# Performance work log

Measured on AMD Instinct MI355X. Metric: run time of the kernel, lower is better.

## Reference

```python
import jax, jax.numpy as jnp
from jax import lax
import numpy as np

B, CIN, HC, K, REC = 64, 64, 64, 3, 5
MG = 240 // REC  # 48
EPS = 1e-8


def conv2d(x, w, b, pad):
    y = lax.conv_general_dilated(x, w, (1, 1), [(pad, pad), (pad, pad)],
                                 dimension_numbers=('NCHW', 'OIHW', 'NCHW'))
    return y + b[None, :, None, None]


def conv_transpose2d(x, w, b, stride, pad):
    # PyTorch ConvTranspose2d: w is (Cin, Cout, kH, kW)
    k = w.shape[2]
    w_t = jnp.transpose(w[:, :, ::-1, ::-1], (1, 0, 2, 3))  # -> OIHW, flipped
    y = lax.conv_general_dilated(x, w_t, (1, 1),
                                 [(k - 1 - pad, k - 1 - pad)] * 2,
                                 lhs_dilation=(stride, stride),
                                 dimension_numbers=('NCHW', 'OIHW', 'NCHW'))
    return y + b[None, :, None, None]


def leaky(x):
    return jnp.where(x >= 0, x, 0.2 * x)


def setup_inputs() -> dict:
    key = jax.random.key(0)
    ks = jax.random.split(key, 12)
    s = 0.05
    return {
        'x': jax.random.normal(ks[0], (B, CIN, 64, 64), jnp.float32),
        'h': jax.random.normal(ks[1], (B, HC, 64, 64), jnp.float32),
        'c': jax.random.normal(ks[2], (B, HC, 64, 64), jnp.float32),
        'recalled_memory_feature': jax.random.normal(ks[3], (B, REC, MG, 32, 32), jnp.float32),
        'conv_w': jax.random.normal(ks[4], (5 * HC, CIN + HC, K, K), jnp.float32) * s,
        'conv_b': jax.random.normal(ks[5], (5 * HC,), jnp.float32) * s,
        'convc_w': jax.random.normal(ks[6], (MG, HC, 1, 1), jnp.float32) * s,
        'convc_b': jax.random.normal(ks[7], (MG,), jnp.float32) * s,
        'convssm_w': jax.random.normal(ks[8], (MG, MG, 4, 4), jnp.float32) * s,
        'convssm_b': jax.random.normal(ks[9], (MG,), jnp.float32) * s,
        'convfuse_w': jax.random.normal(ks[10], (HC, MG + HC, 1, 1), jnp.float32) * s,
        'convfuse_b': jax.random.normal(ks[11], (HC,), jnp.float32) * s,
    }


def reference(x, h, c, recalled_memory_feature, conv_w, conv_b, convc_w, convc_b,
              convssm_w, convssm_b, convfuse_w, convfuse_b):
    rm = recalled_memory_feature.reshape(B, REC, MG, 32, 32)
    rm_avg = rm.mean(axis=(3, 4))                      # (B, REC, MG)
    q = leaky(conv2d(c, convc_w, convc_b, 0))          # (B, MG, 64, 64)
    q_avg = q.mean(axis=(2, 3))                        # (B, MG)
    # cosine similarity along channel dim, vectorized over (B, REC)
    qn = jnp.maximum(jnp.linalg.norm(q_avg, axis=1, keepdims=True), EPS)   # (B,1)
    mn = jnp.maximum(jnp.linalg.norm(rm_avg, axis=2), EPS)                  # (B,REC)
    cos = jnp.einsum('bm,brm->br', q_avg, rm_avg) / (qn * mn)               # (B,REC)
    attn = jax.nn.softmax(cos, axis=1)                                      # (B,REC)
    mt = jnp.einsum('br,brmhw->bmhw', attn, rm)        # (B, MG, 32, 32)
    mt = leaky(conv_transpose2d(mt, convssm_w, convssm_b, 2, 1))  # (B, MG, 64, 64)

    gates = conv2d(jnp.concatenate((x, h), axis=1), conv_w, conv_b, K // 2)
    i, f, g, o, lam = jnp.split(gates, 5, axis=1)
    i = jax.nn.sigmoid(i)
    f = jax.nn.sigmoid(f)
    o = jax.nn.sigmoid(o)
    g = jnp.tanh(g)
    lam = jax.nn.sigmoid(lam)
    c_new = f * c + i * g
    h_new = o * jnp.tanh(conv2d(jnp.concatenate((c_new, mt), axis=1), convfuse_w, convfuse_b, 0))
    h_out = lam * h_new + (1.0 - lam) * h
    return (h_out, c_new)
```

## Files before the change

### kernel.cpp

```cpp
#include <hip/hip_runtime.h>
#include <hip/hip_bf16.h>
#include <cstdint>

#define HW 4096
#define MGc 48
#define RECc 5

typedef __attribute__((ext_vector_type(8))) short bf16x8;
typedef __attribute__((ext_vector_type(4))) float f32x4;

__device__ __forceinline__ float sigf(float x) { return 1.f / (1.f + expf(-x)); }
__device__ __forceinline__ float leakyf(float x) { return x >= 0.f ? x : 0.2f * x; }
__device__ __forceinline__ unsigned short f2bfu(float f) {
  __hip_bfloat16 b = __float2bfloat16(f);
  return *reinterpret_cast<unsigned short*>(&b);
}
__device__ __forceinline__ float bfu2f(unsigned short u) {
  unsigned v = ((unsigned)u) << 16;
  return __uint_as_float(v);
}
__device__ __forceinline__ void gload_lds16(const void* g, void* l) {
  __builtin_amdgcn_global_load_lds(
      (const __attribute__((address_space(1))) unsigned int*)g,
      (__attribute__((address_space(3))) unsigned int*)l, 16, 0, 0);
}

__global__ __launch_bounds__(256) void k_head(const float* __restrict__ cw,
    __hip_bfloat16* __restrict__ Wp, __hip_bfloat16* __restrict__ Pp,
    const float* __restrict__ xin, const float* __restrict__ hin,
    const float* __restrict__ rm, float* __restrict__ rm_sum,
    const float* __restrict__ c, const float* __restrict__ ccw,
    const float* __restrict__ ccb, float* __restrict__ q_part) {
  __shared__ __align__(16) char smem[16704];
  int bid = blockIdx.x;
  int tid = threadIdx.x;
  if (bid < 1440) {
    int idx = bid * 256 + tid;
    int t = idx / (320 * 128);
    int rem = idx % (320 * 128);
    int ocp = rem / 128, ci = rem % 128;
    int nt = ocp / 80, r2 = ocp % 80, gate = r2 / 16, ml = r2 % 16;
    int oc = gate * 64 + nt * 16 + ml;
    Wp[idx] = __float2bfloat16(cw[((size_t)oc * 128 + ci) * 9 + t]);
  } else if (bid < 2480) {
    int idx = (bid - 1440) * 256 + tid;
    int b = idx / 4160, i = idx % 4160;
    bf16x8* base = reinterpret_cast<bf16x8*>(Pp);
    size_t u;
    if (i < 2112) {
      int r = (i < 1056) ? 0 : 65;
      int j = (i < 1056) ? i : i - 1056;
      u = ((size_t)b * 66 + r) * 1056 + j;
    } else {
      int i2 = i - 2112;
      int row = 1 + (i2 >> 5), k = i2 & 31;
      int px = (k < 16) ? 0 : 65, ci8 = k & 15;
      u = (((size_t)b * 66 + row) * 66 + px) * 16 + ci8;
    }
    base[u] = (bf16x8)0;
  } else if (bid < 10672) {
    float (*t)[65] = (float(*)[65])smem;
    int r = bid - 2480;
    int half = r & 1, y = (r >> 1) & 63, b = r >> 7;
    const float* src = (half ? hin : xin) + (size_t)b * 64 * HW + y * 64;
    #pragma unroll
    for (int it = 0; it < 4; it++) {
      int li = it * 256 + tid;
      int ci = li >> 4, x4 = (li & 15) * 4;
      float4 v = *reinterpret_cast<const float4*>(src + (size_t)ci * HW + x4);
      t[x4][ci] = v.x; t[x4 + 1][ci] = v.y; t[x4 + 2][ci] = v.z; t[x4 + 3][ci] = v.w;
    }
    __syncthreads();
    int x = tid >> 2, c16 = (tid & 3) * 16;
    unsigned short* dst = reinterpret_cast<unsigned short*>(Pp) +
        ((((size_t)b * 66 + y + 1) * 66 + x + 1) * 128 + half * 64 + c16);
    bf16x8 o0, o1;
    #pragma unroll
    for (int j = 0; j < 8; j++) {
      o0[j] = (short)f2bfu(t[x][c16 + j]);
      o1[j] = (short)f2bfu(t[x][c16 + 8 + j]);
    }
    *reinterpret_cast<bf16x8*>(dst) = o0;
    *reinterpret_cast<bf16x8*>(dst + 8) = o1;
  } else if (bid < 26032) {
    float* sred = (float*)smem;
    int row = bid - 10672;
    const float4* p = reinterpret_cast<const float4*>(rm + (size_t)row * 1024);
    float4 v = p[tid];
    float s = v.x + v.y + v.z + v.w;
    #pragma unroll
    for (int off = 32; off; off >>= 1) s += __shfl_down(s, off);
    if ((tid & 63) == 0) sred[tid >> 6] = s;
    __syncthreads();
    if (tid == 0) rm_sum[row] = sred[0] + sred[1] + sred[2] + sred[3];
  } else {
    float* wl = (float*)smem;
    float* bl = wl + MGc * 64;
    float (*red)[MGc] = (float(*)[MGc])(bl + 64);
    int r = bid - 26032;
    int seg = r & 15, b = r >> 4;
    for (int i = tid; i < MGc * 64; i += 256) wl[i] = ccw[i];
    if (tid < MGc) bl[tid] = ccb[tid];
    __syncthreads();
    int px = seg * 256 + tid;
    float acc[MGc];
    #pragma unroll
    for (int m = 0; m < MGc; m++) acc[m] = 0.f;
    const float* cp = c + (size_t)b * 64 * HW + px;
    for (int ci = 0; ci < 64; ci++) {
      float v = cp[(size_t)ci * HW];
      #pragma unroll
      for (int m = 0; m < MGc; m++) acc[m] += wl[m * 64 + ci] * v;
    }
    int lane = tid & 63, wv = tid >> 6;
    #pragma unroll
    for (int m = 0; m < MGc; m++) {
      float t2 = leakyf(acc[m] + bl[m]);
      #pragma unroll
      for (int off = 32; off; off >>= 1) t2 += __shfl_down(t2, off);
      if (lane == 0) red[wv][m] = t2;
    }
    __syncthreads();
    if (tid < MGc) {
      float t2 = red[0][tid] + red[1][tid] + red[2][tid] + red[3][tid];
      q_part[((size_t)b * 16 + seg) * MGc + tid] = t2;
    }
  }
}

__global__ __launch_bounds__(256) void k_mt_pre(const float* __restrict__ rm,
    const float* __restrict__ rm_sum, const float* __restrict__ q_part,
    float* __restrict__ mt_pre) {
  __shared__ float sat[RECc];
  int idx = blockIdx.x * 256 + threadIdx.x;
  int b = idx / (MGc * 1024);
  if (threadIdx.x < 64) {
    int lane = threadIdx.x;
    float q = 0.f;
    if (lane < MGc) {
      float s = 0.f;
      for (int sg = 0; sg < 16; sg++) s += q_part[((size_t)b * 16 + sg) * MGc + lane];
      q = s * (1.f / 4096.f);
    }
    float qs = q * q;
    #pragma unroll
    for (int off = 32; off; off >>= 1) qs += __shfl_xor(qs, off);
    float qn = fmaxf(sqrtf(qs), 1e-8f);
    float cosv[RECc];
    #pragma unroll
    for (int r = 0; r < RECc; r++) {
      float m = 0.f;
      if (lane < MGc) m = rm_sum[((size_t)b * RECc + r) * MGc + lane] * (1.f / 1024.f);
      float d = q * m, ms = m * m;
      #pragma unroll
      for (int off = 32; off; off >>= 1) { d += __shfl_xor(d, off); ms += __shfl_xor(ms, off); }
      float mn = fmaxf(sqrtf(ms), 1e-8f);
      cosv[r] = d / (qn * mn);
    }
    float mx = cosv[0];
    #pragma unroll
    for (int r = 1; r < RECc; r++) mx = fmaxf(mx, cosv[r]);
    float ssum = 0.f;
    #pragma unroll
    for (int r = 0; r < RECc; r++) { cosv[r] = expf(cosv[r] - mx); ssum += cosv[r]; }
    float inv = 1.f / ssum;
    #pragma unroll
    for (int r = 0; r < RECc; r++)
      if (lane == r) sat[r] = cosv[r] * inv;
  }
  __syncthreads();
  int rem = idx - b * (MGc * 1024);
  const float* base = rm + (size_t)b * RECc * MGc * 1024 + rem;
  float v = sat[0] * base[0] + sat[1] * base[MGc * 1024] + sat[2] * base[2 * MGc * 1024]
          + sat[3] * base[3 * MGc * 1024] + sat[4] * base[4 * MGc * 1024];
  mt_pre[idx] = v;
}

__global__ __launch_bounds__(512) void k_ssm(const float* __restrict__ mt_pre,
    const float* __restrict__ w, const float* __restrict__ bias,
    __hip_bfloat16* __restrict__ mt) {
  __shared__ float in_t[12][10][20];
  __shared__ float w_t[12][48][16];
  int b = blockIdx.y;
  int tile = blockIdx.x;
  int y0 = (tile >> 1) * 16, x0 = (tile & 1) * 32;
  int wv = threadIdx.x >> 6, lane = threadIdx.x & 63;
  int co0 = wv * 6;
  int oyl = lane >> 2, xseg = lane & 3;
  int oy = y0 + oyl;
  int iy0 = (y0 >> 1) - 1, ix0 = (x0 >> 1) - 1;
  int kyA = (oy + 1) & 1;
  int iyA = (oy + 1 - kyA) >> 1;
  int rA = iyA - iy0, rB = rA - 1;
  float acc[6][8] = {};
  for (int ch = 0; ch < 4; ch++) {
    int ci0 = ch * 12;
    __syncthreads();
    for (int i = threadIdx.x; i < 12 * 10 * 18; i += 512) {
      int ci = i / 180, rr = (i % 180) / 18, cc2 = i % 18;
      int giy = iy0 + rr, gix = ix0 + cc2;
      float v = 0.f;
      if ((unsigned)giy < 32u && (unsigned)gix < 32u)
        v = mt_pre[(((size_t)b * MGc + ci0 + ci) * 32 + giy) * 32 + gix];
      in_t[ci][rr][cc2] = v;
    }
    for (int i = threadIdx.x; i < 12 * 48 * 16; i += 512)
      (&w_t[0][0][0])[i] = w[ci0 * 768 + i];
    __syncthreads();
    #pragma unroll 1
    for (int ci = 0; ci < 12; ci++) {
      float4 a0 = *reinterpret_cast<const float4*>(&in_t[ci][rA][xseg * 4]);
      float4 a1 = *reinterpret_cast<const float4*>(&in_t[ci][rA][xseg * 4 + 4]);
      float4 b0 = *reinterpret_cast<const float4*>(&in_t[ci][rB][xseg * 4]);
      float4 b1 = *reinterpret_cast<const float4*>(&in_t[ci][rB][xseg * 4 + 4]);
      float vA[6] = {a0.x, a0.y, a0.z, a0.w, a1.x, a1.y};
      float vB[6] = {b0.x, b0.y, b0.z, b0.w, b1.x, b1.y};
      #pragma unroll
      for (int co = 0; co < 6; co++) {
        const float* wp = &w_t[ci][co0 + co][0];
        float4 wA = *reinterpret_cast<const float4*>(wp + kyA * 4);
        float4 wB = *reinterpret_cast<const float4*>(wp + (kyA + 2) * 4);
        #pragma unroll
        for (int j = 0; j < 8; j++) {
          if ((j & 1) == 0) {
            int hi = (j >> 1) + 1, lo = j >> 1;
            acc[co][j] += vA[hi] * wA.y + vA[lo] * wA.w + vB[hi] * wB.y + vB[lo] * wB.w;
          } else {
            int hi = ((j + 1) >> 1) + 1, lo = (j + 1) >> 1;
            acc[co][j] += vA[hi] * wA.x + vA[lo] * wA.z + vB[hi] * wB.x + vB[lo] * wB.z;
          }
        }
      }
    }
  }
  int oxb = x0 + xseg * 8;
  #pragma unroll
  for (int co = 0; co < 6; co++) {
    float bb = bias[co0 + co];
    size_t obase = (((size_t)b * MGc + co0 + co) * 64 + oy) * 64 + oxb;
    #pragma unroll
    for (int j = 0; j < 8; j++)
      mt[obase + j] = __float2bfloat16(leakyf(acc[co][j] + bb));
  }
}

__global__ __launch_bounds__(256) void k_gates_mfma(
    const __hip_bfloat16* __restrict__ Pp, const __hip_bfloat16* __restrict__ Wp,
    const float* __restrict__ c, const float* __restrict__ cb,
    float* __restrict__ c_new, __hip_bfloat16* __restrict__ o_g,
    __hip_bfloat16* __restrict__ lam_g) {
  __shared__ bf16x8 s_in[18 * 4 * 18];
  __shared__ bf16x8 s_w[9 * 4 * 80];
  int orig = blockIdx.y * gridDim.x + blockIdx.x;
  int t_id = (orig & 7) * 512 + (orig >> 3);
  int b = t_id >> 6;
  int r6 = t_id & 63;
  int ytile = r6 >> 4, xtile = (r6 >> 2) & 3, nt = r6 & 3;
  int y0 = ytile * 16, x0 = xtile * 16;
  int tid = threadIdx.x;
  int wv = tid >> 6, lane = tid & 63;
  int lane15 = lane & 15, lq = lane >> 4;

  const char* Pb = (const char*)Pp;
  const char* Wb = (const char*)Wp;

  const char* gin[6]; int din[6]; bool ain[6];
  #pragma unroll
  for (int k = 0; k < 6; k++) {
    int u = wv + 4 * k;
    int e = u * 64 + lane;
    ain[k] = (u < 21) && (e < 1296);
    int ee = (e < 1296) ? e : 0;
    int L = ee / 72, r = ee - L * 72;
    int llq = r / 18, xi = r - llq * 18;
    gin[k] = Pb + ((((size_t)b * 66 + y0 + L) * 66 + (x0 + xi)) * 256) + llq * 16;
    din[k] = ee;
  }
  const char* gw[12]; int dw[12]; bool aw[12];
  #pragma unroll
  for (int k = 0; k < 12; k++) {
    int u = wv + 4 * k;
    aw[k] = (u < 45);
    int uu = (u < 45) ? u : 0;
    int e = uu * 64 + lane;
    int unit = e / 80, ol = e - unit * 80;
    int t = unit >> 2, g = unit & 3;
    gw[k] = Wb + (((size_t)t * 320 + nt * 80 + ol) * 128 + g * 8) * 2;
    dw[k] = e;
  }

  f32x4 acc[4][5];
  #pragma unroll
  for (int i = 0; i < 4; i++)
    #pragma unroll
    for (int j = 0; j < 5; j++) acc[i][j] = (f32x4)0.f;

  #pragma unroll 1
  for (int cc = 0; cc < 4; cc++) {
    __syncthreads();
    int co = cc * 64;
    #pragma unroll
    for (int k = 0; k < 6; k++)
      if (ain[k]) gload_lds16(gin[k] + co, (void*)&s_in[din[k]]);
    #pragma unroll
    for (int k = 0; k < 12; k++)
      if (aw[k]) gload_lds16(gw[k] + co, (void*)&s_w[dw[k]]);
    __syncthreads();

    #pragma unroll
    for (int dx = 0; dx < 3; dx++) {
      bf16x8 af[6];
      #pragma unroll
      for (int r = 0; r < 6; r++)
        af[r] = s_in[((wv * 4 + r) * 4 + lq) * 18 + lane15 + dx];
      #pragma unroll
      for (int ky = 0; ky < 3; ky++) {
        int t = ky * 3 + dx;
        bf16x8 bw[5];
        #pragma unroll
        for (int gg = 0; gg < 5; gg++)
          bw[gg] = s_w[(t * 4 + lq) * 80 + gg * 16 + lane15];
        __builtin_amdgcn_s_setprio(1);
        #pragma unroll
        for (int rr = 0; rr < 4; rr++)
          #pragma unroll
          for (int gg = 0; gg < 5; gg++)
            acc[rr][gg] = __builtin_amdgcn_mfma_f32_16x16x32_bf16(
                af[rr + ky], bw[gg], acc[rr][gg], 0, 0, 0);
        __builtin_amdgcn_s_setprio(0);
      }
    }
  }

  int m_hid = nt * 16 + lane15;
  float bi = cb[m_hid], bff = cb[64 + m_hid], bgg = cb[128 + m_hid],
        bo = cb[192 + m_hid], bl = cb[256 + m_hid];
  int xb = x0 + lq * 4;
  size_t chofs = ((size_t)b * 64 + m_hid) * HW;
  #pragma unroll
  for (int rr = 0; rr < 4; rr++) {
    int y = y0 + wv * 4 + rr;
    size_t pofs = chofs + (size_t)y * 64 + xb;
    f32x4 cold = *reinterpret_cast<const f32x4*>(c + pofs);
    f32x4 cn;
    unsigned short ov[4], lv[4];
    #pragma unroll
    for (int e = 0; e < 4; e++) {
      float i_ = sigf(acc[rr][0][e] + bi);
      float f_ = sigf(acc[rr][1][e] + bff);
      float g_ = tanhf(acc[rr][2][e] + bgg);
      float o_ = sigf(acc[rr][3][e] + bo);
      float l_ = sigf(acc[rr][4][e] + bl);
      cn[e] = f_ * cold[e] + i_ * g_;
      ov[e] = f2bfu(o_);
      lv[e] = f2bfu(l_);
    }
    *reinterpret_cast<f32x4*>(c_new + pofs) = cn;
    ushort4 ovv = {ov[0], ov[1], ov[2], ov[3]};
    ushort4 lvv = {lv[0], lv[1], lv[2], lv[3]};
    *reinterpret_cast<ushort4*>(reinterpret_cast<unsigned short*>(o_g) + pofs) = ovv;
    *reinterpret_cast<ushort4*>(reinterpret_cast<unsigned short*>(lam_g) + pofs) = lvv;
  }
}

__global__ __launch_bounds__(256) void k_fuse(const float* __restrict__ c_new,
    const __hip_bfloat16* __restrict__ mt, const __hip_bfloat16* __restrict__ o_g,
    const __hip_bfloat16* __restrict__ lam_g, const float* __restrict__ h,
    const float* __restrict__ fw, const float* __restrict__ fb,
    float* __restrict__ h_out) {
  __shared__ float wl[112][64];
  int b = blockIdx.y, seg = blockIdx.x;
  for (int i = threadIdx.x; i < 112 * 64; i += 256) {
    int ci = i >> 6, co = i & 63;
    wl[ci][co] = fw[co * 112 + ci];
  }
  __syncthreads();
  int px = seg * 512 + threadIdx.x * 2;
  size_t bofs = (size_t)b * 64 * HW;
  float2 acc[64];
  #pragma unroll
  for (int co = 0; co < 64; co++) { float bv = fb[co]; acc[co].x = bv; acc[co].y = bv; }
  #pragma unroll 1
  for (int ci = 0; ci < 64; ci++) {
    float2 v = *reinterpret_cast<const float2*>(c_new + bofs + (size_t)ci * HW + px);
    #pragma unroll
    for (int c4 = 0; c4 < 16; c4++) {
      float4 w = *reinterpret_cast<const float4*>(&wl[ci][c4 * 4]);
      acc[c4 * 4 + 0].x += w.x * v.x; acc[c4 * 4 + 0].y += w.x * v.y;
      acc[c4 * 4 + 1].x += w.y * v.x; acc[c4 * 4 + 1].y += w.y * v.y;
      acc[c4 * 4 + 2].x += w.z * v.x; acc[c4 * 4 + 2].y += w.z * v.y;
      acc[c4 * 4 + 3].x += w.w * v.x; acc[c4 * 4 + 3].y += w.w * v.y;
    }
  }
  const unsigned short* mtu = reinterpret_cast<const unsigned short*>(mt);
  size_t mtofs = (size_t)b * MGc * HW + px;
  #pragma unroll 1
  for (int ci = 0; ci < 48; ci++) {
    unsigned u = *reinterpret_cast<const unsigned*>(mtu + mtofs + (size_t)ci * HW);
    float vx = bfu2f((unsigned short)(u & 0xffff));
    float vy = bfu2f((unsigned short)(u >> 16));
    #pragma unroll
    for (int c4 = 0; c4 < 16; c4++) {
      float4 w = *reinterpret_cast<const float4*>(&wl[64 + ci][c4 * 4]);
      acc[c4 * 4 + 0].x += w.x * vx; acc[c4 * 4 + 0].y += w.x * vy;
      acc[c4 * 4 + 1].x += w.y * vx; acc[c4 * 4 + 1].y += w.y * vy;
      acc[c4 * 4 + 2].x += w.z * vx; acc[c4 * 4 + 2].y += w.z * vy;
      acc[c4 * 4 + 3].x += w.w * vx; acc[c4 * 4 + 3].y += w.w * vy;
    }
  }
  const unsigned short* ou = reinterpret_cast<const unsigned short*>(o_g);
  const unsigned short* lu = reinterpret_cast<const unsigned short*>(lam_g);
  #pragma unroll
  for (int co = 0; co < 64; co++) {
    size_t ofs = bofs + (size_t)co * HW + px;
    unsigned uo = *reinterpret_cast<const unsigned*>(ou + ofs);
    unsigned ul = *reinterpret_cast<const unsigned*>(lu + ofs);
    float2 hv = *reinterpret_cast<const float2*>(h + ofs);
    float hnx = tanhf(acc[co].x), hny = tanhf(acc[co].y);
    float ox = bfu2f((unsigned short)(uo & 0xffff)), oy = bfu2f((unsigned short)(uo >> 16));
    float lx = bfu2f((unsigned short)(ul & 0xffff)), ly = bfu2f((unsigned short)(ul >> 16));
    float2 r;
    r.x = lx * (ox * hnx) + (1.f - lx) * hv.x;
    r.y = ly * (oy * hny) + (1.f - ly) * hv.y;
    *reinterpret_cast<float2*>(h_out + ofs) = r;
  }
}

extern "C" void kernel_launch(void* const* d_in, const int* in_sizes, int n_in,
                              void* d_out, int out_size, void* d_ws, size_t ws_size,
                              hipStream_t stream) {
  const float* x   = (const float*)d_in[0];
  const float* h   = (const float*)d_in[1];
  const float* c   = (const float*)d_in[2];
  const float* rm  = (const float*)d_in[3];
  const float* cw  = (const float*)d_in[4];
  const float* cb  = (const float*)d_in[5];
  const float* ccw = (const float*)d_in[6];
  const float* ccb = (const float*)d_in[7];
  const float* sw  = (const float*)d_in[8];
  const float* sb  = (const float*)d_in[9];
  const float* fw  = (const float*)d_in[10];
  const float* fb  = (const float*)d_in[11];

  float* h_out = (float*)d_out;
  float* c_new = h_out + (size_t)16777216;

  char* ws = (char*)d_ws;
  float* rm_sum = (float*)(ws + 0);
  float* q_part = (float*)(ws + 65536);
  float* mt_pre = (float*)(ws + 262144);
  __hip_bfloat16* o_g   = (__hip_bfloat16*)(ws + 0);
  __hip_bfloat16* lam_g = (__hip_bfloat16*)(ws + 33554432);
  __hip_bfloat16* mt    = (__hip_bfloat16*)(ws + 67108864);
  __hip_bfloat16* Pp    = (__hip_bfloat16*)(ws + 92274688);
  __hip_bfloat16* Wp    = (__hip_bfloat16*)(ws + 163643392);

  k_head<<<27056, 256, 0, stream>>>(cw, Wp, Pp, x, h, rm, rm_sum, c, ccw, ccb, q_part);
  k_mt_pre<<<12288, 256, 0, stream>>>(rm, rm_sum, q_part, mt_pre);
  k_ssm<<<dim3(8, 64), 512, 0, stream>>>(mt_pre, sw, sb, mt);
  k_gates_mfma<<<dim3(64, 64), 256, 0, stream>>>(Pp, Wp, c, cb, c_new, o_g, lam_g);
  k_fuse<<<dim3(8, 64), 256, 0, stream>>>(c_new, mt, o_g, lam_g, h, fw, fb, h_out);
}
```

Baseline: 655.9 us.

## Rebalance kernel partitioning, pad gate weight LDS rows, split fuse output channels

Regroups the head work into two launches: a small attention-statistics kernel, then a combined kernel that does the mt_pre weighting alongside weight and input packing. The combined launch removes the separate mt_pre kernel and lets those independent jobs overlap. The gates MFMA kernel pads its LDS weight rows from 80 to 81 entries to cut bank conflicts. The fuse kernel now splits its 64 output channels across two blocks, halving per-thread accumulators to raise occupancy, but each block re-reads the inputs. mt_pre now lives in the h_out buffer, which relies on k_fuse overwriting it later.

```diff
diff --git a/kernel.cpp b/kernel.cpp
--- a/kernel.cpp
+++ b/kernel.cpp
@@ -25,25 +25,119 @@
       (__attribute__((address_space(3))) unsigned int*)l, 16, 0, 0);
 }
 
-__global__ __launch_bounds__(256) void k_head(const float* __restrict__ cw,
+__global__ __launch_bounds__(256) void k_att(const float* __restrict__ rm,
+    float* __restrict__ rm_sum, const float* __restrict__ c,
+    const float* __restrict__ ccw, const float* __restrict__ ccb,
+    float* __restrict__ q_part) {
+  __shared__ __align__(16) char smem[13568];
+  int bid = blockIdx.x, tid = threadIdx.x;
+  if (bid < 15360) {
+    float* sred = (float*)smem;
+    int row = bid;
+    const float4* p = reinterpret_cast<const float4*>(rm + (size_t)row * 1024);
+    float4 v = p[tid];
+    float s = v.x + v.y + v.z + v.w;
+    #pragma unroll
+    for (int off = 32; off; off >>= 1) s += __shfl_down(s, off);
+    if ((tid & 63) == 0) sred[tid >> 6] = s;
+    __syncthreads();
+    if (tid == 0) rm_sum[row] = sred[0] + sred[1] + sred[2] + sred[3];
+  } else {
+    float* wl = (float*)smem;
+    float* bl = wl + MGc * 64;
+    float (*red)[MGc] = (float(*)[MGc])(bl + 64);
+    int r = bid - 15360;
+    int seg = r & 15, b = r >> 4;
+    for (int i = tid; i < MGc * 64; i += 256) wl[i] = ccw[i];
+    if (tid < MGc) bl[tid] = ccb[tid];
+    __syncthreads();
+    int px = seg * 256 + tid;
+    float acc[MGc];
+    #pragma unroll
+    for (int m = 0; m < MGc; m++) acc[m] = 0.f;
+    const float* cp = c + (size_t)b * 64 * HW + px;
+    for (int ci = 0; ci < 64; ci++) {
+      float v = cp[(size_t)ci * HW];
+      #pragma unroll
+      for (int m = 0; m < MGc; m++) acc[m] += wl[m * 64 + ci] * v;
+    }
+    int lane = tid & 63, wv = tid >> 6;
+    #pragma unroll
+    for (int m = 0; m < MGc; m++) {
+      float t2 = leakyf(acc[m] + bl[m]);
+      #pragma unroll
+      for (int off = 32; off; off >>= 1) t2 += __shfl_down(t2, off);
+      if (lane == 0) red[wv][m] = t2;
+    }
+    __syncthreads();
+    if (tid < MGc) {
+      float t2 = red[0][tid] + red[1][tid] + red[2][tid] + red[3][tid];
+      q_part[((size_t)b * 16 + seg) * MGc + tid] = t2;
+    }
+  }
+}
+
+__global__ __launch_bounds__(256) void k_mid(const float* __restrict__ rm,
+    const float* __restrict__ rm_sum, const float* __restrict__ q_part,
+    float* __restrict__ mt_pre, const float* __restrict__ cw,
     __hip_bfloat16* __restrict__ Wp, __hip_bfloat16* __restrict__ Pp,
-    const float* __restrict__ xin, const float* __restrict__ hin,
-    const float* __restrict__ rm, float* __restrict__ rm_sum,
-    const float* __restrict__ c, const float* __restrict__ ccw,
-    const float* __restrict__ ccb, float* __restrict__ q_part) {
+    const float* __restrict__ xin, const float* __restrict__ hin) {
   __shared__ __align__(16) char smem[16704];
-  int bid = blockIdx.x;
-  int tid = threadIdx.x;
-  if (bid < 1440) {
+  int bid = blockIdx.x, tid = threadIdx.x;
+  if (bid < 12288) {
+    float* sat = (float*)smem;
     int idx = bid * 256 + tid;
+    int b = idx / (MGc * 1024);
+    if (tid < 64) {
+      int lane = tid;
+      float q = 0.f;
+      if (lane < MGc) {
+        float s = 0.f;
+        for (int sg = 0; sg < 16; sg++) s += q_part[((size_t)b * 16 + sg) * MGc + lane];
+        q = s * (1.f / 4096.f);
+      }
+      float qs = q * q;
+      #pragma unroll
+      for (int off = 32; off; off >>= 1) qs += __shfl_xor(qs, off);
+      float qn = fmaxf(sqrtf(qs), 1e-8f);
+      float cosv[RECc];
+      #pragma unroll
+      for (int r = 0; r < RECc; r++) {
+        float m = 0.f;
+        if (lane < MGc) m = rm_sum[((size_t)b * RECc + r) * MGc + lane] * (1.f / 1024.f);
+        float d = q * m, ms = m * m;
+        #pragma unroll
+        for (int off = 32; off; off >>= 1) { d += __shfl_xor(d, off); ms += __shfl_xor(ms, off); }
+        float mn = fmaxf(sqrtf(ms), 1e-8f);
+        cosv[r] = d / (qn * mn);
+      }
+      float mx = cosv[0];
+      #pragma unroll
+      for (int r = 1; r < RECc; r++) mx = fmaxf(mx, cosv[r]);
+      float ssum = 0.f;
+      #pragma unroll
+      for (int r = 0; r < RECc; r++) { cosv[r] = expf(cosv[r] - mx); ssum += cosv[r]; }
+      float inv = 1.f / ssum;
+      #pragma unroll
+      for (int r = 0; r < RECc; r++)
+        if (lane == r) sat[r] = cosv[r] * inv;
+    }
+    __syncthreads();
+    int rem = idx - b * (MGc * 1024);
+    const float* base = rm + (size_t)b * RECc * MGc * 1024 + rem;
+    float v = sat[0] * base[0] + sat[1] * base[MGc * 1024] + sat[2] * base[2 * MGc * 1024]
+            + sat[3] * base[3 * MGc * 1024] + sat[4] * base[4 * MGc * 1024];
+    mt_pre[idx] = v;
+  } else if (bid < 13728) {
+    int idx = (bid - 12288) * 256 + tid;
     int t = idx / (320 * 128);
     int rem = idx % (320 * 128);
     int ocp = rem / 128, ci = rem % 128;
     int nt = ocp / 80, r2 = ocp % 80, gate = r2 / 16, ml = r2 % 16;
     int oc = gate * 64 + nt * 16 + ml;
     Wp[idx] = __float2bfloat16(cw[((size_t)oc * 128 + ci) * 9 + t]);
-  } else if (bid < 2480) {
-    int idx = (bid - 1440) * 256 + tid;
+  } else if (bid < 14768) {
+    int idx = (bid - 13728) * 256 + tid;
     int b = idx / 4160, i = idx % 4160;
     bf16x8* base = reinterpret_cast<bf16x8*>(Pp);
     size_t u;
@@ -58,9 +152,9 @@
       u = (((size_t)b * 66 + row) * 66 + px) * 16 + ci8;
     }
     base[u] = (bf16x8)0;
-  } else if (bid < 10672) {
+  } else {
     float (*t)[65] = (float(*)[65])smem;
-    int r = bid - 2480;
+    int r = bid - 14768;
     int half = r & 1, y = (r >> 1) & 63, b = r >> 7;
     const float* src = (half ? hin : xin) + (size_t)b * 64 * HW + y * 64;
     #pragma unroll
@@ -82,98 +176,7 @@
     }
     *reinterpret_cast<bf16x8*>(dst) = o0;
     *reinterpret_cast<bf16x8*>(dst + 8) = o1;
-  } else if (bid < 26032) {
-    float* sred = (float*)smem;
-    int row = bid - 10672;
-    const float4* p = reinterpret_cast<const float4*>(rm + (size_t)row * 1024);
-    float4 v = p[tid];
-    float s = v.x + v.y + v.z + v.w;
-    #pragma unroll
-    for (int off = 32; off; off >>= 1) s += __shfl_down(s, off);
-    if ((tid & 63) == 0) sred[tid >> 6] = s;
-    __syncthreads();
-    if (tid == 0) rm_sum[row] = sred[0] + sred[1] + sred[2] + sred[3];
-  } else {
-    float* wl = (float*)smem;
-    float* bl = wl + MGc * 64;
-    float (*red)[MGc] = (float(*)[MGc])(bl + 64);
-    int r = bid - 26032;
-    int seg = r & 15, b = r >> 4;
-    for (int i = tid; i < MGc * 64; i += 256) wl[i] = ccw[i];
-    if (tid < MGc) bl[tid] = ccb[tid];
-    __syncthreads();
-    int px = seg * 256 + tid;
-    float acc[MGc];
-    #pragma unroll
-    for (int m = 0; m < MGc; m++) acc[m] = 0.f;
-    const float* cp = c + (size_t)b * 64 * HW + px;
-    for (int ci = 0; ci < 64; ci++) {
-      float v = cp[(size_t)ci * HW];
-      #pragma unroll
-      for (int m = 0; m < MGc; m++) acc[m] += wl[m * 64 + ci] * v;
-    }
-    int lane = tid & 63, wv = tid >> 6;
-    #pragma unroll
-    for (int m = 0; m < MGc; m++) {
-      float t2 = leakyf(acc[m] + bl[m]);
-      #pragma unroll
-      for (int off = 32; off; off >>= 1) t2 += __shfl_down(t2, off);
-      if (lane == 0) red[wv][m] = t2;
-    }
-    __syncthreads();
-    if (tid < MGc) {
-      float t2 = red[0][tid] + red[1][tid] + red[2][tid] + red[3][tid];
-      q_part[((size_t)b * 16 + seg) * MGc + tid] = t2;
-    }
-  }
-}
-
-__global__ __launch_bounds__(256) void k_mt_pre(const float* __restrict__ rm,
-    const float* __restrict__ rm_sum, const float* __restrict__ q_part,
-    float* __restrict__ mt_pre) {
-  __shared__ float sat[RECc];
-  int idx = blockIdx.x * 256 + threadIdx.x;
-  int b = idx / (MGc * 1024);
-  if (threadIdx.x < 64) {
-    int lane = threadIdx.x;
-    float q = 0.f;
-    if (lane < MGc) {
-      float s = 0.f;
-      for (int sg = 0; sg < 16; sg++) s += q_part[((size_t)b * 16 + sg) * MGc + lane];
-      q = s * (1.f / 4096.f);
-    }
-    float qs = q * q;
-    #pragma unroll
-    for (int off = 32; off; off >>= 1) qs += __shfl_xor(qs, off);
-    float qn = fmaxf(sqrtf(qs), 1e-8f);
-    float cosv[RECc];
-    #pragma unroll
-    for (int r = 0; r < RECc; r++) {
-      float m = 0.f;
-      if (lane < MGc) m = rm_sum[((size_t)b * RECc + r) * MGc + lane] * (1.f / 1024.f);
-      float d = q * m, ms = m * m;
-      #pragma unroll
-      for (int off = 32; off; off >>= 1) { d += __shfl_xor(d, off); ms += __shfl_xor(ms, off); }
-      float mn = fmaxf(sqrtf(ms), 1e-8f);
-      cosv[r] = d / (qn * mn);
-    }
-    float mx = cosv[0];
-    #pragma unroll
-    for (int r = 1; r < RECc; r++) mx = fmaxf(mx, cosv[r]);
-    float ssum = 0.f;
-    #pragma unroll
-    for (int r = 0; r < RECc; r++) { cosv[r] = expf(cosv[r] - mx); ssum += cosv[r]; }
-    float inv = 1.f / ssum;
-    #pragma unroll
-    for (int r = 0; r < RECc; r++)
-      if (lane == r) sat[r] = cosv[r] * inv;
-  }
-  __syncthreads();
-  int rem = idx - b * (MGc * 1024);
-  const float* base = rm + (size_t)b * RECc * MGc * 1024 + rem;
-  float v = sat[0] * base[0] + sat[1] * base[MGc * 1024] + sat[2] * base[2 * MGc * 1024]
-          + sat[3] * base[3 * MGc * 1024] + sat[4] * base[4 * MGc * 1024];
-  mt_pre[idx] = v;
+  }
 }
 
 __global__ __launch_bounds__(512) void k_ssm(const float* __restrict__ mt_pre,
@@ -249,8 +252,8 @@
     const float* __restrict__ c, const float* __restrict__ cb,
     float* __restrict__ c_new, __hip_bfloat16* __restrict__ o_g,
     __hip_bfloat16* __restrict__ lam_g) {
-  __shared__ bf16x8 s_in[18 * 4 * 18];
-  __shared__ bf16x8 s_w[9 * 4 * 80];
+  __shared__ bf16x8 s_in[1296];
+  __shared__ bf16x8 s_w[2944];
   int orig = blockIdx.y * gridDim.x + blockIdx.x;
   int t_id = (orig & 7) * 512 + (orig >> 3);
   int b = t_id >> 6;
@@ -280,13 +283,14 @@
   #pragma unroll
   for (int k = 0; k < 12; k++) {
     int u = wv + 4 * k;
-    aw[k] = (u < 45);
-    int uu = (u < 45) ? u : 0;
-    int e = uu * 64 + lane;
-    int unit = e / 80, ol = e - unit * 80;
-    int t = unit >> 2, g = unit & 3;
+    int e = u * 64 + lane;
+    aw[k] = (e < 2916);
+    int ee = aw[k] ? e : 0;
+    int row = ee / 81, ol = ee - row * 81;
+    if (ol > 79) ol = 0;
+    int t = row >> 2, g = row & 3;
     gw[k] = Wb + (((size_t)t * 320 + nt * 80 + ol) * 128 + g * 8) * 2;
-    dw[k] = e;
+    dw[k] = ee;
   }
 
   f32x4 acc[4][5];
@@ -319,7 +323,7 @@
         bf16x8 bw[5];
         #pragma unroll
         for (int gg = 0; gg < 5; gg++)
-          bw[gg] = s_w[(t * 4 + lq) * 80 + gg * 16 + lane15];
+          bw[gg] = s_w[(t * 4 + lq) * 81 + gg * 16 + lane15];
         __builtin_amdgcn_s_setprio(1);
         #pragma unroll
         for (int rr = 0; rr < 4; rr++)
@@ -368,23 +372,25 @@
     const __hip_bfloat16* __restrict__ lam_g, const float* __restrict__ h,
     const float* __restrict__ fw, const float* __restrict__ fb,
     float* __restrict__ h_out) {
-  __shared__ float wl[112][64];
-  int b = blockIdx.y, seg = blockIdx.x;
-  for (int i = threadIdx.x; i < 112 * 64; i += 256) {
-    int ci = i >> 6, co = i & 63;
-    wl[ci][co] = fw[co * 112 + ci];
+  __shared__ float wl[112][32];
+  int b = blockIdx.y;
+  int seg = blockIdx.x & 7, chalf = blockIdx.x >> 3;
+  int co0 = chalf * 32;
+  for (int i = threadIdx.x; i < 112 * 32; i += 256) {
+    int ci = i >> 5, co = i & 31;
+    wl[ci][co] = fw[(co0 + co) * 112 + ci];
   }
   __syncthreads();
   int px = seg * 512 + threadIdx.x * 2;
   size_t bofs = (size_t)b * 64 * HW;
-  float2 acc[64];
-  #pragma unroll
-  for (int co = 0; co < 64; co++) { float bv = fb[co]; acc[co].x = bv; acc[co].y = bv; }
+  float2 acc[32];
+  #pragma unroll
+  for (int co = 0; co < 32; co++) { float bv = fb[co0 + co]; acc[co].x = bv; acc[co].y = bv; }
   #pragma unroll 1
   for (int ci = 0; ci < 64; ci++) {
     float2 v = *reinterpret_cast<const float2*>(c_new + bofs + (size_t)ci * HW + px);
     #pragma unroll
-    for (int c4 = 0; c4 < 16; c4++) {
+    for (int c4 = 0; c4 < 8; c4++) {
       float4 w = *reinterpret_cast<const float4*>(&wl[ci][c4 * 4]);
       acc[c4 * 4 + 0].x += w.x * v.x; acc[c4 * 4 + 0].y += w.x * v.y;
       acc[c4 * 4 + 1].x += w.y * v.x; acc[c4 * 4 + 1].y += w.y * v.y;
@@ -400,7 +406,7 @@
     float vx = bfu2f((unsigned short)(u & 0xffff));
     float vy = bfu2f((unsigned short)(u >> 16));
     #pragma unroll
-    for (int c4 = 0; c4 < 16; c4++) {
+    for (int c4 = 0; c4 < 8; c4++) {
       float4 w = *reinterpret_cast<const float4*>(&wl[64 + ci][c4 * 4]);
       acc[c4 * 4 + 0].x += w.x * vx; acc[c4 * 4 + 0].y += w.x * vy;
       acc[c4 * 4 + 1].x += w.y * vx; acc[c4 * 4 + 1].y += w.y * vy;
@@ -411,8 +417,8 @@
   const unsigned short* ou = reinterpret_cast<const unsigned short*>(o_g);
   const unsigned short* lu = reinterpret_cast<const unsigned short*>(lam_g);
   #pragma unroll
-  for (int co = 0; co < 64; co++) {
-    size_t ofs = bofs + (size_t)co * HW + px;
+  for (int co = 0; co < 32; co++) {
+    size_t ofs = bofs + (size_t)(co0 + co) * HW + px;
     unsigned uo = *reinterpret_cast<const unsigned*>(ou + ofs);
     unsigned ul = *reinterpret_cast<const unsigned*>(lu + ofs);
     float2 hv = *reinterpret_cast<const float2*>(h + ofs);
@@ -448,16 +454,16 @@
   char* ws = (char*)d_ws;
   float* rm_sum = (float*)(ws + 0);
   float* q_part = (float*)(ws + 65536);
-  float* mt_pre = (float*)(ws + 262144);
   __hip_bfloat16* o_g   = (__hip_bfloat16*)(ws + 0);
   __hip_bfloat16* lam_g = (__hip_bfloat16*)(ws + 33554432);
   __hip_bfloat16* mt    = (__hip_bfloat16*)(ws + 67108864);
   __hip_bfloat16* Pp    = (__hip_bfloat16*)(ws + 92274688);
   __hip_bfloat16* Wp    = (__hip_bfloat16*)(ws + 163643392);
-
-  k_head<<<27056, 256, 0, stream>>>(cw, Wp, Pp, x, h, rm, rm_sum, c, ccw, ccb, q_part);
-  k_mt_pre<<<12288, 256, 0, stream>>>(rm, rm_sum, q_part, mt_pre);
+  float* mt_pre = h_out;
+
+  k_att<<<16384, 256, 0, stream>>>(rm, rm_sum, c, ccw, ccb, q_part);
+  k_mid<<<22960, 256, 0, stream>>>(rm, rm_sum, q_part, mt_pre, cw, Wp, Pp, x, h);
   k_ssm<<<dim3(8, 64), 512, 0, stream>>>(mt_pre, sw, sb, mt);
   k_gates_mfma<<<dim3(64, 64), 256, 0, stream>>>(Pp, Wp, c, cb, c_new, o_g, lam_g);
-  k_fuse<<<dim3(8, 64), 256, 0, stream>>>(c_new, mt, o_g, lam_g, h, fw, fb, h_out);
-}
+  k_fuse<<<dim3(16, 64), 256, 0, stream>>>(c_new, mt, o_g, lam_g, h, fw, fb, h_out);
+}
```

Measured after the change: 641.4 us. -2.2%, faster.
